# Optimization experiments

Hardware: AMD Instinct MI355X
Metric: run time of the kernel (lower is better)

## Reference

```python
import jax, jax.numpy as jnp
import numpy as np
from jax import lax

B, T = 64, 2048
ENC, DEC, ATT = 512, 1024, 128
NFILT, KSIZE = 32, 31
PAD = KSIZE // 2


def setup_inputs() -> dict:
    key = jax.random.key(0)
    ks = jax.random.split(key, 9)
    query = jax.random.normal(ks[0], (B, 1, DEC), dtype=jnp.float32)
    keys = jax.random.normal(ks[1], (B, T, ENC), dtype=jnp.float32)
    prev_weights = jax.random.uniform(ks[2], (B, T), dtype=jnp.float32)
    mask = jax.random.randint(ks[3], (B, T), 0, 2, dtype=jnp.int32)
    # params stored as [in, out] (transpose of torch Linear weight); same math
    W1 = jax.random.normal(ks[4], (ENC, ATT), dtype=jnp.float32) * (ENC ** -0.5)
    W2 = jax.random.normal(ks[5], (DEC, ATT), dtype=jnp.float32) * (DEC ** -0.5)
    V = jax.random.normal(ks[6], (ATT,), dtype=jnp.float32) * (ATT ** -0.5)
    conv_w = jax.random.normal(ks[7], (NFILT, 1, KSIZE), dtype=jnp.float32) * (KSIZE ** -0.5)
    loc_dense = jax.random.normal(ks[8], (NFILT, ATT), dtype=jnp.float32) * (NFILT ** -0.5)
    return {"query": query, "keys": keys, "prev_weights": prev_weights, "mask": mask,
            "W1": W1, "W2": W2, "V": V, "conv_w": conv_w, "loc_dense": loc_dense}


def reference(query, keys, prev_weights, mask, W1, W2, V, conv_w, loc_dense):
    proj_key = jnp.einsum('bte,ea->bta', keys, W1)          # [B,T,A]
    proj_query = jnp.einsum('bqd,da->bqa', query, W2)       # [B,1,A]
    # location conv: input [B,1,T], kernel [F,1,K], 'same' padding -> [B,F,T]
    loc_feat = lax.conv_general_dilated(prev_weights[:, None, :], conv_w,
                                        window_strides=(1,), padding=[(PAD, PAD)],
                                        dimension_numbers=('NCH', 'OIH', 'NCH'))
    proj_loc = jnp.einsum('bft,fa->bta', loc_feat, loc_dense)  # [B,T,A]
    scores = jnp.einsum('bta,a->bt', jnp.tanh(proj_key + proj_query + proj_loc), V)
    scores = jnp.where(mask == 0, -1e9, scores)
    weights = jax.nn.softmax(scores, axis=-1)                # [B,T]
    context = jnp.einsum('bt,bte->be', weights, keys)[:, None, :]  # [B,1,ENC]
    return context, weights
```

## Files before the change

### kernel.cpp

```cpp
#include <hip/hip_runtime.h>

typedef __attribute__((ext_vector_type(4))) float f32x4;
typedef __attribute__((ext_vector_type(8))) short bf16x8;

#define T_LEN 2048
#define ENC   512
#define DEC   1024
#define ATT   128
#define NB    64
#define BM    256
#define NTB   (T_LEN / BM)
#define NSTEP 17

typedef unsigned int u32;
typedef __attribute__((address_space(1))) const u32 gu32;
typedef __attribute__((address_space(3))) u32 lu32;

__device__ __forceinline__ void async_copy16(const void* g, void* l) {
  __builtin_amdgcn_global_load_lds((gu32*)g, (lu32*)l, 16, 0, 0);
}

__device__ __forceinline__ unsigned short f2bf_rne(float x) {
  unsigned int u = __builtin_bit_cast(unsigned int, x);
  u += 0x7fff + ((u >> 16) & 1);
  return (unsigned short)(u >> 16);
}
__device__ __forceinline__ short f2bf_fast(float x) {
  unsigned int u = __builtin_bit_cast(unsigned int, x);
  return (short)((u + 0x8000u) >> 16);
}

__device__ __forceinline__ float fast_tanh(float x) {
  float e = __expf(2.f * x);
  return 1.f - 2.f / (e + 1.f);
}

__global__ __launch_bounds__(128) void prep(
    const float* __restrict__ query, const float* __restrict__ W2,
    const float* __restrict__ W1, const float* __restrict__ convw,
    const float* __restrict__ ldense,
    float* __restrict__ pq, unsigned short* __restrict__ Bl) {
  int bidx = blockIdx.x;
  if (bidx < NB) {
    int a = threadIdx.x;
    const float* q = query + bidx * DEC;
    float a0 = 0.f, a1 = 0.f, a2 = 0.f, a3 = 0.f;
    for (int d = 0; d < DEC; d += 4) {
      a0 += q[d]     * W2[(d)     * ATT + a];
      a1 += q[d + 1] * W2[(d + 1) * ATT + a];
      a2 += q[d + 2] * W2[(d + 2) * ATT + a];
      a3 += q[d + 3] * W2[(d + 3) * ATT + a];
    }
    pq[bidx * ATT + a] = (a0 + a1) + (a2 + a3);
  } else {
    int a = bidx - NB;
    int n = a >> 4, rs = a & 15;
    for (int k = threadIdx.x; k < NSTEP * 32; k += 128) {
      float v = 0.f;
      if (k < 512) {
        v = W1[k * ATT + a];
      } else if (k < 543) {
        int kc = k - 512;
        #pragma unroll
        for (int f = 0; f < 32; ++f) v += convw[f * 31 + kc] * ldense[f * ATT + a];
      }
      int t = k >> 5, g = (k & 31) >> 3, j = k & 7;
      Bl[(((t * 8 + n) * 64 + g * 16 + rs) << 3) + j] = f2bf_rne(v);
    }
  }
}

__global__ __launch_bounds__(512, 1) void lsa_main(
    const float* __restrict__ keys, const float* __restrict__ prev,
    const int* __restrict__ mask, const unsigned short* __restrict__ Bl,
    const float* __restrict__ pq, const float* __restrict__ Vv,
    float* __restrict__ wout, float* __restrict__ dpart, float* __restrict__ cpart) {
  __shared__ unsigned short Bsh[NSTEP * 4096];
  __shared__ float e_vals[BM];

  const int tid = threadIdx.x;
  const int bid = blockIdx.x;
  const int b = bid >> 3;
  const int trow0 = (bid & 7) * BM;
  const int lane = tid & 63;
  const int w = tid >> 6;
  const int rsel = lane & 15, grp = lane >> 4;
  const int row0 = trow0 + w * 32;

  const float* keyrow = keys + ((size_t)b * T_LEN + row0 + rsel) * ENC + grp * 8;

  f32x4 acc[2][8];
  #pragma unroll
  for (int m = 0; m < 2; ++m)
    #pragma unroll
    for (int n = 0; n < 8; ++n) acc[m][n] = (f32x4)0.f;

  f32x4 A0, A1, A2, A3, B0, B1, B2, B3, C0, C1, C2, C3;

#define LOADK(S, t_) do { \
    S##0 = *(const f32x4*)(keyrow + (t_) * 32); \
    S##1 = *(const f32x4*)(keyrow + (t_) * 32 + 4); \
    S##2 = *(const f32x4*)(keyrow + 16 * ENC + (t_) * 32); \
    S##3 = *(const f32x4*)(keyrow + 16 * ENC + (t_) * 32 + 4); } while (0)

#define LOADP(S) do { \
    _Pragma("unroll") \
    for (int j_ = 0; j_ < 4; ++j_) { \
      int kk0 = grp * 8 + j_, kk1 = grp * 8 + 4 + j_; \
      int p00 = row0 + rsel + kk0 - 15, p01 = row0 + rsel + kk1 - 15; \
      S##0[j_] = (kk0 < 31 && p00 >= 0 && p00 < T_LEN) ? prev[b * T_LEN + p00] : 0.f; \
      S##1[j_] = (kk1 < 31 && p01 >= 0 && p01 < T_LEN) ? prev[b * T_LEN + p01] : 0.f; \
      S##2[j_] = (kk0 < 31 && p00 + 16 >= 0 && p00 + 16 < T_LEN) ? prev[b * T_LEN + p00 + 16] : 0.f; \
      S##3[j_] = (kk1 < 31 && p01 + 16 >= 0 && p01 + 16 < T_LEN) ? prev[b * T_LEN + p01 + 16] : 0.f; \
    } } while (0)

#define STEP(t_, S) do { \
    bf16x8 af0, af1; \
    _Pragma("unroll") \
    for (int j_ = 0; j_ < 4; ++j_) { \
      af0[j_] = f2bf_fast(S##0[j_]); af0[4 + j_] = f2bf_fast(S##1[j_]); \
      af1[j_] = f2bf_fast(S##2[j_]); af1[4 + j_] = f2bf_fast(S##3[j_]); \
    } \
    const unsigned short* Bt_ = &Bsh[(t_) * 4096]; \
    _Pragma("unroll") \
    for (int n_ = 0; n_ < 8; ++n_) { \
      bf16x8 bf_ = *(const bf16x8*)(Bt_ + n_ * 512 + lane * 8); \
      acc[0][n_] = __builtin_amdgcn_mfma_f32_16x16x32_bf16(af0, bf_, acc[0][n_], 0, 0, 0); \
      acc[1][n_] = __builtin_amdgcn_mfma_f32_16x16x32_bf16(af1, bf_, acc[1][n_], 0, 0, 0); \
    } } while (0)

  LOADK(A, 0);
  LOADK(B, 1);
  {
    const char* src = (const char*)Bl + w * 1024 + lane * 16;
    char* dst = (char*)Bsh + w * 1024;
    #pragma unroll
    for (int s = 0; s < NSTEP; ++s)
      async_copy16(src + s * 8192, dst + s * 8192);
  }
  __syncthreads();

  LOADK(C, 2);  STEP(0, A);
  LOADK(A, 3);  STEP(1, B);
  LOADK(B, 4);  STEP(2, C);
  LOADK(C, 5);  STEP(3, A);
  LOADK(A, 6);  STEP(4, B);
  LOADK(B, 7);  STEP(5, C);
  LOADK(C, 8);  STEP(6, A);
  LOADK(A, 9);  STEP(7, B);
  LOADK(B, 10); STEP(8, C);
  LOADK(C, 11); STEP(9, A);
  LOADK(A, 12); STEP(10, B);
  LOADK(B, 13); STEP(11, C);
  LOADK(C, 14); STEP(12, A);
  LOADK(A, 15); STEP(13, B);
  LOADP(B);     STEP(14, C);
  STEP(15, A);
  STEP(16, B);

  float psum[2][4];
  #pragma unroll
  for (int m = 0; m < 2; ++m)
    #pragma unroll
    for (int i = 0; i < 4; ++i) psum[m][i] = 0.f;
  #pragma unroll
  for (int n = 0; n < 8; ++n) {
    int c = n * 16 + rsel;
    float pqv = pq[b * ATT + c];
    float vv = Vv[c];
    #pragma unroll
    for (int m = 0; m < 2; ++m)
      #pragma unroll
      for (int i = 0; i < 4; ++i)
        psum[m][i] += vv * fast_tanh(acc[m][n][i] + pqv);
  }
  #pragma unroll
  for (int m = 0; m < 2; ++m)
    #pragma unroll
    for (int i = 0; i < 4; ++i) {
      float v = psum[m][i];
      v += __shfl_xor(v, 1, 64);
      v += __shfl_xor(v, 2, 64);
      v += __shfl_xor(v, 4, 64);
      v += __shfl_xor(v, 8, 64);
      psum[m][i] = v;
    }
  if (rsel == 0) {
    #pragma unroll
    for (int m = 0; m < 2; ++m)
      #pragma unroll
      for (int i = 0; i < 4; ++i) {
        int r = w * 32 + m * 16 + grp * 4 + i;
        int gr = b * T_LEN + trow0 + r;
        float e = (mask[gr] == 0) ? 0.f : __expf(psum[m][i]);
        wout[gr] = e;
        e_vals[r] = e;
      }
  }
  __syncthreads();

  if (tid < 64) {
    float v = e_vals[tid] + e_vals[tid + 64] + e_vals[tid + 128] + e_vals[tid + 192];
    #pragma unroll
    for (int off = 32; off; off >>= 1) v += __shfl_xor(v, off, 64);
    if (tid == 0) dpart[bid] = v;
  }

  {
    const float* kb = keys + ((size_t)b * T_LEN + trow0) * ENC + tid;
    float c0 = 0.f, c1 = 0.f, c2 = 0.f, c3 = 0.f;
    #pragma unroll 4
    for (int r = 0; r < BM; r += 4) {
      c0 += e_vals[r]     * kb[(size_t)(r)     * ENC];
      c1 += e_vals[r + 1] * kb[(size_t)(r + 1) * ENC];
      c2 += e_vals[r + 2] * kb[(size_t)(r + 2) * ENC];
      c3 += e_vals[r + 3] * kb[(size_t)(r + 3) * ENC];
    }
    cpart[(size_t)bid * ENC + tid] = (c0 + c1) + (c2 + c3);
  }
}

__global__ __launch_bounds__(256) void lsa_finalize(
    const float* __restrict__ dpart, const float* __restrict__ cpart,
    float* __restrict__ out) {
  int b = blockIdx.x, tid = threadIdx.x;
  float d = 0.f;
  #pragma unroll
  for (int i = 0; i < NTB; ++i) d += dpart[b * NTB + i];
  float inv = 1.f / d;
  for (int e = tid; e < ENC; e += 256) {
    float c = 0.f;
    #pragma unroll
    for (int i = 0; i < NTB; ++i) c += cpart[((size_t)(b * NTB + i)) * ENC + e];
    out[b * ENC + e] = c * inv;
  }
  float* wrow = out + NB * ENC + (size_t)b * T_LEN;
  for (int t = tid; t < T_LEN; t += 256) wrow[t] *= inv;
}

extern "C" void kernel_launch(void* const* d_in, const int* in_sizes, int n_in,
                              void* d_out, int out_size, void* d_ws, size_t ws_size,
                              hipStream_t stream) {
  const float* query  = (const float*)d_in[0];
  const float* keys   = (const float*)d_in[1];
  const float* prev   = (const float*)d_in[2];
  const int*   mask   = (const int*)d_in[3];
  const float* W1     = (const float*)d_in[4];
  const float* W2     = (const float*)d_in[5];
  const float* V      = (const float*)d_in[6];
  const float* convw  = (const float*)d_in[7];
  const float* ldense = (const float*)d_in[8];
  float* out = (float*)d_out;

  char* ws = (char*)d_ws;
  unsigned short* Bl = (unsigned short*)ws;
  float* pq    = (float*)(ws + 139264);
  float* dpart = (float*)(ws + 139264 + 32768);
  float* cpart = (float*)(ws + 139264 + 32768 + 4096);

  prep<<<dim3(192), dim3(128), 0, stream>>>(query, W2, W1, convw, ldense, pq, Bl);
  lsa_main<<<dim3(NB * NTB), dim3(512), 0, stream>>>(keys, prev, mask, Bl, pq, V,
                                                     out + NB * ENC, dpart, cpart);
  lsa_finalize<<<dim3(NB), dim3(256), 0, stream>>>(dpart, cpart, out);
}
```

Before: 137.4 us.

## Use single-wave blocks with register-streamed B tiles instead of LDS staging

The main kernel now launches one 64-thread wave per 32-row tile (4096 blocks) instead of 512-thread blocks covering 256 rows. B weight fragments are read straight from global memory (L2-resident) into double-buffered registers, with no LDS copy or block barrier. The context accumulation skips masked rows and uses vectorized loads. The costs are a larger partial-sum buffer, more work for the finalize kernel (64 partials per batch instead of 8), and more register pressure.

```diff
diff --git a/kernel.cpp b/kernel.cpp
--- a/kernel.cpp
+++ b/kernel.cpp
@@ -8,17 +8,8 @@
 #define DEC   1024
 #define ATT   128
 #define NB    64
-#define BM    256
-#define NTB   (T_LEN / BM)
+#define NTB   64
 #define NSTEP 17
-
-typedef unsigned int u32;
-typedef __attribute__((address_space(1))) const u32 gu32;
-typedef __attribute__((address_space(3))) u32 lu32;
-
-__device__ __forceinline__ void async_copy16(const void* g, void* l) {
-  __builtin_amdgcn_global_load_lds((gu32*)g, (lu32*)l, 16, 0, 0);
-}
 
 __device__ __forceinline__ unsigned short f2bf_rne(float x) {
   unsigned int u = __builtin_bit_cast(unsigned int, x);
@@ -70,24 +61,21 @@
   }
 }
 
-__global__ __launch_bounds__(512, 1) void lsa_main(
+__global__ __launch_bounds__(64, 2) void lsa_main(
     const float* __restrict__ keys, const float* __restrict__ prev,
     const int* __restrict__ mask, const unsigned short* __restrict__ Bl,
     const float* __restrict__ pq, const float* __restrict__ Vv,
     float* __restrict__ wout, float* __restrict__ dpart, float* __restrict__ cpart) {
-  __shared__ unsigned short Bsh[NSTEP * 4096];
-  __shared__ float e_vals[BM];
-
-  const int tid = threadIdx.x;
+  __shared__ float e_vals[32];
+
+  const int lane = threadIdx.x;
   const int bid = blockIdx.x;
-  const int b = bid >> 3;
-  const int trow0 = (bid & 7) * BM;
-  const int lane = tid & 63;
-  const int w = tid >> 6;
+  const int b = bid >> 6;
+  const int row0 = (bid & 63) * 32;
   const int rsel = lane & 15, grp = lane >> 4;
-  const int row0 = trow0 + w * 32;
 
   const float* keyrow = keys + ((size_t)b * T_LEN + row0 + rsel) * ENC + grp * 8;
+  const unsigned short* Bp = Bl + lane * 8;
 
   f32x4 acc[2][8];
   #pragma unroll
@@ -96,6 +84,8 @@
     for (int n = 0; n < 8; ++n) acc[m][n] = (f32x4)0.f;
 
   f32x4 A0, A1, A2, A3, B0, B1, B2, B3, C0, C1, C2, C3;
+  bf16x8 P0, P1, P2, P3, P4, P5, P6, P7;
+  bf16x8 Q0, Q1, Q2, Q3, Q4, Q5, Q6, Q7;
 
 #define LOADK(S, t_) do { \
     S##0 = *(const f32x4*)(keyrow + (t_) * 32); \
@@ -114,49 +104,58 @@
       S##3[j_] = (kk1 < 31 && p01 + 16 >= 0 && p01 + 16 < T_LEN) ? prev[b * T_LEN + p01 + 16] : 0.f; \
     } } while (0)
 
-#define STEP(t_, S) do { \
+#define LOADB(S, t_) do { \
+    S##0 = *(const bf16x8*)(Bp + ((t_) * 8 + 0) * 512); \
+    S##1 = *(const bf16x8*)(Bp + ((t_) * 8 + 1) * 512); \
+    S##2 = *(const bf16x8*)(Bp + ((t_) * 8 + 2) * 512); \
+    S##3 = *(const bf16x8*)(Bp + ((t_) * 8 + 3) * 512); \
+    S##4 = *(const bf16x8*)(Bp + ((t_) * 8 + 4) * 512); \
+    S##5 = *(const bf16x8*)(Bp + ((t_) * 8 + 5) * 512); \
+    S##6 = *(const bf16x8*)(Bp + ((t_) * 8 + 6) * 512); \
+    S##7 = *(const bf16x8*)(Bp + ((t_) * 8 + 7) * 512); } while (0)
+
+#define STEP(S, BB) do { \
     bf16x8 af0, af1; \
     _Pragma("unroll") \
     for (int j_ = 0; j_ < 4; ++j_) { \
       af0[j_] = f2bf_fast(S##0[j_]); af0[4 + j_] = f2bf_fast(S##1[j_]); \
       af1[j_] = f2bf_fast(S##2[j_]); af1[4 + j_] = f2bf_fast(S##3[j_]); \
     } \
-    const unsigned short* Bt_ = &Bsh[(t_) * 4096]; \
-    _Pragma("unroll") \
-    for (int n_ = 0; n_ < 8; ++n_) { \
-      bf16x8 bf_ = *(const bf16x8*)(Bt_ + n_ * 512 + lane * 8); \
-      acc[0][n_] = __builtin_amdgcn_mfma_f32_16x16x32_bf16(af0, bf_, acc[0][n_], 0, 0, 0); \
-      acc[1][n_] = __builtin_amdgcn_mfma_f32_16x16x32_bf16(af1, bf_, acc[1][n_], 0, 0, 0); \
-    } } while (0)
-
-  LOADK(A, 0);
-  LOADK(B, 1);
-  {
-    const char* src = (const char*)Bl + w * 1024 + lane * 16;
-    char* dst = (char*)Bsh + w * 1024;
-    #pragma unroll
-    for (int s = 0; s < NSTEP; ++s)
-      async_copy16(src + s * 8192, dst + s * 8192);
-  }
-  __syncthreads();
-
-  LOADK(C, 2);  STEP(0, A);
-  LOADK(A, 3);  STEP(1, B);
-  LOADK(B, 4);  STEP(2, C);
-  LOADK(C, 5);  STEP(3, A);
-  LOADK(A, 6);  STEP(4, B);
-  LOADK(B, 7);  STEP(5, C);
-  LOADK(C, 8);  STEP(6, A);
-  LOADK(A, 9);  STEP(7, B);
-  LOADK(B, 10); STEP(8, C);
-  LOADK(C, 11); STEP(9, A);
-  LOADK(A, 12); STEP(10, B);
-  LOADK(B, 13); STEP(11, C);
-  LOADK(C, 14); STEP(12, A);
-  LOADK(A, 15); STEP(13, B);
-  LOADP(B);     STEP(14, C);
-  STEP(15, A);
-  STEP(16, B);
+    acc[0][0] = __builtin_amdgcn_mfma_f32_16x16x32_bf16(af0, BB##0, acc[0][0], 0, 0, 0); \
+    acc[1][0] = __builtin_amdgcn_mfma_f32_16x16x32_bf16(af1, BB##0, acc[1][0], 0, 0, 0); \
+    acc[0][1] = __builtin_amdgcn_mfma_f32_16x16x32_bf16(af0, BB##1, acc[0][1], 0, 0, 0); \
+    acc[1][1] = __builtin_amdgcn_mfma_f32_16x16x32_bf16(af1, BB##1, acc[1][1], 0, 0, 0); \
+    acc[0][2] = __builtin_amdgcn_mfma_f32_16x16x32_bf16(af0, BB##2, acc[0][2], 0, 0, 0); \
+    acc[1][2] = __builtin_amdgcn_mfma_f32_16x16x32_bf16(af1, BB##2, acc[1][2], 0, 0, 0); \
+    acc[0][3] = __builtin_amdgcn_mfma_f32_16x16x32_bf16(af0, BB##3, acc[0][3], 0, 0, 0); \
+    acc[1][3] = __builtin_amdgcn_mfma_f32_16x16x32_bf16(af1, BB##3, acc[1][3], 0, 0, 0); \
+    acc[0][4] = __builtin_amdgcn_mfma_f32_16x16x32_bf16(af0, BB##4, acc[0][4], 0, 0, 0); \
+    acc[1][4] = __builtin_amdgcn_mfma_f32_16x16x32_bf16(af1, BB##4, acc[1][4], 0, 0, 0); \
+    acc[0][5] = __builtin_amdgcn_mfma_f32_16x16x32_bf16(af0, BB##5, acc[0][5], 0, 0, 0); \
+    acc[1][5] = __builtin_amdgcn_mfma_f32_16x16x32_bf16(af1, BB##5, acc[1][5], 0, 0, 0); \
+    acc[0][6] = __builtin_amdgcn_mfma_f32_16x16x32_bf16(af0, BB##6, acc[0][6], 0, 0, 0); \
+    acc[1][6] = __builtin_amdgcn_mfma_f32_16x16x32_bf16(af1, BB##6, acc[1][6], 0, 0, 0); \
+    acc[0][7] = __builtin_amdgcn_mfma_f32_16x16x32_bf16(af0, BB##7, acc[0][7], 0, 0, 0); \
+    acc[1][7] = __builtin_amdgcn_mfma_f32_16x16x32_bf16(af1, BB##7, acc[1][7], 0, 0, 0); } while (0)
+
+  LOADK(A, 0); LOADK(B, 1); LOADB(P, 0);
+  LOADK(C, 2);  LOADB(Q, 1);  STEP(A, P);
+  LOADK(A, 3);  LOADB(P, 2);  STEP(B, Q);
+  LOADK(B, 4);  LOADB(Q, 3);  STEP(C, P);
+  LOADK(C, 5);  LOADB(P, 4);  STEP(A, Q);
+  LOADK(A, 6);  LOADB(Q, 5);  STEP(B, P);
+  LOADK(B, 7);  LOADB(P, 6);  STEP(C, Q);
+  LOADK(C, 8);  LOADB(Q, 7);  STEP(A, P);
+  LOADK(A, 9);  LOADB(P, 8);  STEP(B, Q);
+  LOADK(B, 10); LOADB(Q, 9);  STEP(C, P);
+  LOADK(C, 11); LOADB(P, 10); STEP(A, Q);
+  LOADK(A, 12); LOADB(Q, 11); STEP(B, P);
+  LOADK(B, 13); LOADB(P, 12); STEP(C, Q);
+  LOADK(C, 14); LOADB(Q, 13); STEP(A, P);
+  LOADK(A, 15); LOADB(P, 14); STEP(B, Q);
+  LOADP(B);     LOADB(Q, 15); STEP(C, P);
+  LOADB(P, 16); STEP(A, Q);
+  STEP(B, P);
 
   float psum[2][4];
   #pragma unroll
@@ -185,38 +184,40 @@
       v += __shfl_xor(v, 8, 64);
       psum[m][i] = v;
     }
+  float esum = 0.f;
   if (rsel == 0) {
     #pragma unroll
     for (int m = 0; m < 2; ++m)
       #pragma unroll
       for (int i = 0; i < 4; ++i) {
-        int r = w * 32 + m * 16 + grp * 4 + i;
-        int gr = b * T_LEN + trow0 + r;
+        int r = m * 16 + grp * 4 + i;
+        int gr = b * T_LEN + row0 + r;
         float e = (mask[gr] == 0) ? 0.f : __expf(psum[m][i]);
         wout[gr] = e;
         e_vals[r] = e;
+        esum += e;
       }
   }
+  esum += __shfl_xor(esum, 16, 64);
+  esum += __shfl_xor(esum, 32, 64);
+  if (lane == 0) dpart[bid] = esum;
   __syncthreads();
 
-  if (tid < 64) {
-    float v = e_vals[tid] + e_vals[tid + 64] + e_vals[tid + 128] + e_vals[tid + 192];
-    #pragma unroll
-    for (int off = 32; off; off >>= 1) v += __shfl_xor(v, off, 64);
-    if (tid == 0) dpart[bid] = v;
-  }
-
   {
-    const float* kb = keys + ((size_t)b * T_LEN + trow0) * ENC + tid;
-    float c0 = 0.f, c1 = 0.f, c2 = 0.f, c3 = 0.f;
+    const float* kb = keys + ((size_t)b * T_LEN + row0) * ENC + lane * 8;
+    f32x4 c0 = (f32x4)0.f, c1 = (f32x4)0.f;
     #pragma unroll 4
-    for (int r = 0; r < BM; r += 4) {
-      c0 += e_vals[r]     * kb[(size_t)(r)     * ENC];
-      c1 += e_vals[r + 1] * kb[(size_t)(r + 1) * ENC];
-      c2 += e_vals[r + 2] * kb[(size_t)(r + 2) * ENC];
-      c3 += e_vals[r + 3] * kb[(size_t)(r + 3) * ENC];
-    }
-    cpart[(size_t)bid * ENC + tid] = (c0 + c1) + (c2 + c3);
+    for (int r = 0; r < 32; ++r) {
+      float e = e_vals[r];
+      if (e != 0.f) {
+        f32x4 k0 = *(const f32x4*)(kb + (size_t)r * ENC);
+        f32x4 k1 = *(const f32x4*)(kb + (size_t)r * ENC + 4);
+        c0 += e * k0;
+        c1 += e * k1;
+      }
+    }
+    *(f32x4*)(cpart + (size_t)bid * ENC + lane * 8) = c0;
+    *(f32x4*)(cpart + (size_t)bid * ENC + lane * 8 + 4) = c1;
   }
 }
 
@@ -256,10 +257,10 @@
   unsigned short* Bl = (unsigned short*)ws;
   float* pq    = (float*)(ws + 139264);
   float* dpart = (float*)(ws + 139264 + 32768);
-  float* cpart = (float*)(ws + 139264 + 32768 + 4096);
+  float* cpart = (float*)(ws + 139264 + 32768 + 16384);
 
   prep<<<dim3(192), dim3(128), 0, stream>>>(query, W2, W1, convw, ldense, pq, Bl);
-  lsa_main<<<dim3(NB * NTB), dim3(512), 0, stream>>>(keys, prev, mask, Bl, pq, V,
-                                                     out + NB * ENC, dpart, cpart);
+  lsa_main<<<dim3(NB * NTB), dim3(64), 0, stream>>>(keys, prev, mask, Bl, pq, V,
+                                                    out + NB * ENC, dpart, cpart);
   lsa_finalize<<<dim3(NB), dim3(256), 0, stream>>>(dpart, cpart, out);
 }
```

New measurement: 144.6 us. 1.05x slower.
